# Kernel optimization log

Measured on AMD Instinct MI355X. Metric: run time of the kernel, lower is better.

The kernel has to match this reference:

```python
import jax, jax.numpy as jnp
import numpy as np

N = 8192
D_IN = 512
D_OUT = 64
ALPHA = 0.2  # LeakyReLU negative slope
MASK_VAL = -9e15


def setup_inputs() -> dict:
    key = jax.random.key(0)
    k1, k2, k3, k4 = jax.random.split(key, 4)
    inp = jax.random.normal(k1, (N, D_IN), dtype=jnp.float32)
    adj = (jax.random.uniform(k2, (N, N)) < 0.05).astype(jnp.float32)
    adj = adj.at[jnp.arange(N), jnp.arange(N)].set(1.0)
    W = jax.random.normal(k3, (D_IN, D_OUT), dtype=jnp.float32) * 0.05
    a = jax.random.normal(k4, (2 * D_OUT, 1), dtype=jnp.float32) * 0.05
    return {"input": inp, "adj": adj, "W": W, "a": a}


def reference(input, adj, W, a):
    # h = input @ W : [n, out]
    h = input @ W
    # Algebraic equivalent of the dense pairwise concat:
    # e_ij = leakyrelu([h_i || h_j] . a) = leakyrelu(h_i.a1 + h_j.a2)
    a1, a2 = a[:D_OUT, 0], a[D_OUT:, 0]          # [out], [out]
    e = jax.nn.leaky_relu(
        (h @ a1)[:, None] + (h @ a2)[None, :],    # [n, n]
        negative_slope=ALPHA,
    )
    attention = jnp.where(adj > 0, e, MASK_VAL)
    attention = jax.nn.softmax(attention, axis=1)
    out = attention @ h                            # [n, out]
    return jax.nn.elu(out)                         # end=False branch
```

## Files before the change

kernel.cpp:

```cpp
#include <hip/hip_runtime.h>
#include <hip/hip_bf16.h>

#define N 8192
#define D_IN 512
#define D_OUT 64
#define ALPHA 0.2f
#define BM 64
#define NSPLIT 4
#define KSEG (N / NSPLIT)
#define NSH (KSEG / 128)
#define NSLICE (NSPLIT * 4)

typedef __attribute__((ext_vector_type(4))) float f32x4;
typedef __attribute__((ext_vector_type(8))) short bf16x8;

static __device__ __forceinline__ unsigned pk_bf16(float lo, float hi) {
    unsigned ulo = __bfloat16_as_ushort(__float2bfloat16(lo));
    unsigned uhi = __bfloat16_as_ushort(__float2bfloat16(hi));
    return (uhi << 16) | ulo;
}

__global__ __launch_bounds__(256) void gat_mask_kernel(
    const float* __restrict__ adj, unsigned char* __restrict__ msk)
{
    size_t wave = ((size_t)blockIdx.x * 256 + threadIdx.x) >> 6;
    int lane = threadIdx.x & 63;
#pragma unroll
    for (int it = 0; it < 8; ++it) {
        size_t fo = (wave * 8 + it) * 512 + (size_t)lane * 8;
        float4 v0 = *(const float4*)(adj + fo);
        float4 v1 = *(const float4*)(adj + fo + 4);
        unsigned b =  (unsigned)(v0.x > 0.f)
                   | ((unsigned)(v0.y > 0.f) << 1)
                   | ((unsigned)(v0.z > 0.f) << 2)
                   | ((unsigned)(v0.w > 0.f) << 3)
                   | ((unsigned)(v1.x > 0.f) << 4)
                   | ((unsigned)(v1.y > 0.f) << 5)
                   | ((unsigned)(v1.z > 0.f) << 6)
                   | ((unsigned)(v1.w > 0.f) << 7);
        msk[fo >> 3] = (unsigned char)b;
    }
}

__global__ __launch_bounds__(256) void gat_h_kernel(
    const float* __restrict__ input, const float* __restrict__ W,
    const float* __restrict__ a, unsigned short* __restrict__ hpk,
    float* __restrict__ s1, float* __restrict__ s2)
{
    __shared__ float hp[4][4][64];
    int ws   = threadIdx.x >> 6;
    int lane = threadIdx.x & 63;
    int row0 = blockIdx.x * 4;
    const float* in0 = input + (size_t)row0 * D_IN + ws * 128;
    const float* Wp  = W + ws * 128 * D_OUT;
    float acc[4] = {0.f, 0.f, 0.f, 0.f};
#pragma unroll 4
    for (int k = 0; k < 128; ++k) {
        float wk = Wp[k * D_OUT + lane];
#pragma unroll
        for (int r = 0; r < 4; ++r)
            acc[r] = fmaf(in0[r * D_IN + k], wk, acc[r]);
    }
#pragma unroll
    for (int r = 0; r < 4; ++r) hp[ws][r][lane] = acc[r];
    __syncthreads();
    if (ws == 0) {
        float h[4];
#pragma unroll
        for (int r = 0; r < 4; ++r)
            h[r] = (hp[0][r][lane] + hp[1][r][lane]) + (hp[2][r][lane] + hp[3][r][lane]);
        int kw = row0 >> 5, kb = (row0 >> 3) & 3, e0 = row0 & 7;
        int dw = lane >> 4, dd = lane & 15;
        size_t off = ((size_t)((kw * 4 + dw) * 64) + kb * 16 + dd) * 8 + e0;
        uint2 hv;
        hv.x = pk_bf16(h[0], h[1]);
        hv.y = pk_bf16(h[2], h[3]);
        *(uint2*)(hpk + off) = hv;
        float a1 = a[lane], a2 = a[D_OUT + lane];
#pragma unroll
        for (int r = 0; r < 4; ++r) {
            float p1 = h[r] * a1;
            float p2 = h[r] * a2;
#pragma unroll
            for (int off2 = 32; off2; off2 >>= 1) {
                p1 += __shfl_xor(p1, off2, 64);
                p2 += __shfl_xor(p2, off2, 64);
            }
            if (lane == 0) { s1[row0 + r] = p1; s2[row0 + r] = p2; }
        }
    }
}

struct MSP { unsigned m[4]; float4 sA, sB; };
struct UBP { uint4 b0, b1, b2, b3; };

static __device__ __forceinline__ void issue_ms(MSP& p,
    const unsigned char* m0, const unsigned char* m1,
    const unsigned char* m2, const unsigned char* m3,
    const float* sb, int ps) {
    p.m[0] = m0[ps * 16];
    p.m[1] = m1[ps * 16];
    p.m[2] = m2[ps * 16];
    p.m[3] = m3[ps * 16];
    p.sA = *(const float4*)(sb + ps * 128);
    p.sB = *(const float4*)(sb + ps * 128 + 4);
}
static __device__ __forceinline__ void issue_ub(UBP& p, const unsigned short* hb,
                                                int ps) {
    const unsigned short* f = hb + ((size_t)ps << 13);
    p.b0 = *(const uint4*)(f);
    p.b1 = *(const uint4*)(f + 512);
    p.b2 = *(const uint4*)(f + 1024);
    p.b3 = *(const uint4*)(f + 1536);
}

__global__ __launch_bounds__(256, 2) void gat_flash_kernel(
    const unsigned char* __restrict__ msk, const unsigned short* __restrict__ hpk,
    const float* __restrict__ s1, const float* __restrict__ s2,
    float* __restrict__ pacc, float* __restrict__ plsum)
{
    const int tid  = threadIdx.x;
    const int lane = tid & 63;
    const int ws   = tid >> 6;
    const int i    = lane & 15;
    const int kb   = lane >> 4;
    const int hf   = blockIdx.x >> 7;
    const int rb   = blockIdx.x & 127;
    const int r0   = rb * BM;

    const unsigned char* mb0 = msk + ((size_t)(r0 +  0 + i) << 10) + hf * 256 + ws * 4 + kb;
    const unsigned char* mb1 = msk + ((size_t)(r0 + 16 + i) << 10) + hf * 256 + ws * 4 + kb;
    const unsigned char* mb2 = msk + ((size_t)(r0 + 32 + i) << 10) + hf * 256 + ws * 4 + kb;
    const unsigned char* mb3 = msk + ((size_t)(r0 + 48 + i) << 10) + hf * 256 + ws * 4 + kb;
    const float* s2b = s2 + hf * KSEG + ws * 32 + kb * 8;
    const unsigned short* hb = hpk + (((size_t)(hf * 64 + ws)) << 11) + (lane << 3);

    float eref[4];
#pragma unroll
    for (int ag = 0; ag < 4; ++ag) {
        int rg = r0 + ag * 16 + i;
        float e = s1[rg] + s2[rg];
        eref[ag] = e > 0.f ? e : ALPHA * e;
    }
    float s1r[4];
#pragma unroll
    for (int ag = 0; ag < 4; ++ag) s1r[ag] = s1[r0 + ag * 16 + i];

    float lsum[4] = {0.f, 0.f, 0.f, 0.f};
    f32x4 acc[4][4];
#pragma unroll
    for (int ag = 0; ag < 4; ++ag)
#pragma unroll
        for (int dw = 0; dw < 4; ++dw) acc[ag][dw] = f32x4{0.f, 0.f, 0.f, 0.f};

    auto step = [&](const MSP& p, const UBP& u) {
        const float* sv0 = (const float*)&p.sA;
        const float* sv1 = (const float*)&p.sB;
        const uint4 ub[4] = {u.b0, u.b1, u.b2, u.b3};
#pragma unroll
        for (int ag = 0; ag < 4; ++ag) {
            float w[8];
#pragma unroll
            for (int z = 0; z < 4; ++z) {
                float e0 = s1r[ag] + sv0[z]; e0 = e0 > 0.f ? e0 : ALPHA * e0;
                float e1 = s1r[ag] + sv1[z]; e1 = e1 > 0.f ? e1 : ALPHA * e1;
                float w0 = __expf(e0 - eref[ag]);
                float w1 = __expf(e1 - eref[ag]);
                w[z]     = ((p.m[ag] >> z) & 1u)       ? w0 : 0.f;
                w[z + 4] = ((p.m[ag] >> (z + 4)) & 1u) ? w1 : 0.f;
            }
#pragma unroll
            for (int z = 0; z < 8; ++z) lsum[ag] += w[z];
            uint4 pk;
            pk.x = pk_bf16(w[0], w[1]); pk.y = pk_bf16(w[2], w[3]);
            pk.z = pk_bf16(w[4], w[5]); pk.w = pk_bf16(w[6], w[7]);
            bf16x8 A = __builtin_bit_cast(bf16x8, pk);
            acc[ag][0] = __builtin_amdgcn_mfma_f32_16x16x32_bf16(A, __builtin_bit_cast(bf16x8, ub[0]), acc[ag][0], 0, 0, 0);
            acc[ag][1] = __builtin_amdgcn_mfma_f32_16x16x32_bf16(A, __builtin_bit_cast(bf16x8, ub[1]), acc[ag][1], 0, 0, 0);
            acc[ag][2] = __builtin_amdgcn_mfma_f32_16x16x32_bf16(A, __builtin_bit_cast(bf16x8, ub[2]), acc[ag][2], 0, 0, 0);
            acc[ag][3] = __builtin_amdgcn_mfma_f32_16x16x32_bf16(A, __builtin_bit_cast(bf16x8, ub[3]), acc[ag][3], 0, 0, 0);
        }
    };

    MSP M0, M1; UBP U0, U1;
    issue_ms(M0, mb0, mb1, mb2, mb3, s2b, 0); issue_ub(U0, hb, 0);
    issue_ms(M1, mb0, mb1, mb2, mb3, s2b, 1); issue_ub(U1, hb, 1);
    for (int p = 0; p < NSH; p += 2) {
        step(M0, U0);
        if (p + 2 < NSH) { issue_ms(M0, mb0, mb1, mb2, mb3, s2b, p + 2); issue_ub(U0, hb, p + 2); }
        step(M1, U1);
        if (p + 3 < NSH) { issue_ms(M1, mb0, mb1, mb2, mb3, s2b, p + 3); issue_ub(U1, hb, p + 3); }
    }

#pragma unroll
    for (int ag = 0; ag < 4; ++ag) {
        lsum[ag] += __shfl_xor(lsum[ag], 16, 64);
        lsum[ag] += __shfl_xor(lsum[ag], 32, 64);
    }
    const int sp = hf * 4 + ws;
    if (lane < 16) {
#pragma unroll
        for (int ag = 0; ag < 4; ++ag)
            plsum[(size_t)sp * N + r0 + ag * 16 + lane] = lsum[ag];
    }
#pragma unroll
    for (int ag = 0; ag < 4; ++ag)
#pragma unroll
        for (int dw = 0; dw < 4; ++dw)
#pragma unroll
            for (int reg = 0; reg < 4; ++reg)
                pacc[((size_t)sp * N + r0 + ag * 16 + kb * 4 + reg) * 64 + dw * 16 + i]
                    = acc[ag][dw][reg];
}

__global__ __launch_bounds__(256) void gat_reduce_kernel(
    const float* __restrict__ pacc, const float* __restrict__ plsum,
    float* __restrict__ out)
{
    int idx = blockIdx.x * 256 + threadIdx.x;
    int row = idx >> 6;
    float aa = 0.f, l = 0.f;
#pragma unroll
    for (int sp = 0; sp < NSLICE; ++sp) {
        aa += pacc[(size_t)sp * N * 64 + idx];
        l  += plsum[(size_t)sp * N + row];
    }
    float o = aa / l;
    out[idx] = o > 0.f ? o : expm1f(o);
}

extern "C" void kernel_launch(void* const* d_in, const int* in_sizes, int n_in,
                              void* d_out, int out_size, void* d_ws, size_t ws_size,
                              hipStream_t stream) {
    const float* input = (const float*)d_in[0];
    const float* adj   = (const float*)d_in[1];
    const float* W     = (const float*)d_in[2];
    const float* a     = (const float*)d_in[3];
    float* out = (float*)d_out;

    unsigned short* hpk = (unsigned short*)d_ws;
    float* s1    = (float*)(hpk + (size_t)N * D_OUT);
    float* s2    = s1 + N;
    float* pacc  = s2 + N;
    float* plsum = pacc + (size_t)NSLICE * N * 64;
    unsigned char* msk = (unsigned char*)(plsum + (size_t)NSLICE * N);

    gat_mask_kernel<<<4096, 256, 0, stream>>>(adj, msk);
    gat_h_kernel<<<2048, 256, 0, stream>>>(input, W, a, hpk, s1, s2);
    gat_flash_kernel<<<128 * NSPLIT, 256, 0, stream>>>(msk, hpk, s1, s2, pacc, plsum);
    gat_reduce_kernel<<<N * 64 / 256, 256, 0, stream>>>(pacc, plsum, out);
}
```

Before: 139.9 us.

## Halve flash row tile, reduce wave partials in LDS, batch mask loads

Shrinks the attention row tile from 64 to 32 rows, doubling the flash grid and raising launch-bound occupancy to 4 blocks per CU. The four per-wave partial accumulators are now summed in shared memory before writing, which cuts partial-sum traffic and the reduce kernel's work from 16 slices to 4. The mask kernel issues all its adjacency loads before computing and writes the mask bytes coalesced. The trade-off is that every block reloads the same h and s2 data for half as many rows, so h traffic through cache doubles, and the block gains an LDS barrier.

Result: slower. 188.7 us (+34.9%).

```diff
diff --git a/kernel.cpp b/kernel.cpp
--- a/kernel.cpp
+++ b/kernel.cpp
@@ -5,11 +5,11 @@
 #define D_IN 512
 #define D_OUT 64
 #define ALPHA 0.2f
-#define BM 64
+#define BM 32
+#define NRB (N / BM)
 #define NSPLIT 4
 #define KSEG (N / NSPLIT)
 #define NSH (KSEG / 128)
-#define NSLICE (NSPLIT * 4)
 
 typedef __attribute__((ext_vector_type(4))) float f32x4;
 typedef __attribute__((ext_vector_type(8))) short bf16x8;
@@ -25,11 +25,17 @@
 {
     size_t wave = ((size_t)blockIdx.x * 256 + threadIdx.x) >> 6;
     int lane = threadIdx.x & 63;
+    const float* base = adj + wave * 4096 + (size_t)lane * 8;
+    float4 v[16];
 #pragma unroll
     for (int it = 0; it < 8; ++it) {
-        size_t fo = (wave * 8 + it) * 512 + (size_t)lane * 8;
-        float4 v0 = *(const float4*)(adj + fo);
-        float4 v1 = *(const float4*)(adj + fo + 4);
+        v[2 * it]     = *(const float4*)(base + it * 512);
+        v[2 * it + 1] = *(const float4*)(base + it * 512 + 4);
+    }
+    size_t bo = wave * 512 + lane;
+#pragma unroll
+    for (int it = 0; it < 8; ++it) {
+        float4 v0 = v[2 * it], v1 = v[2 * it + 1];
         unsigned b =  (unsigned)(v0.x > 0.f)
                    | ((unsigned)(v0.y > 0.f) << 1)
                    | ((unsigned)(v0.z > 0.f) << 2)
@@ -38,7 +44,7 @@
                    | ((unsigned)(v1.y > 0.f) << 5)
                    | ((unsigned)(v1.z > 0.f) << 6)
                    | ((unsigned)(v1.w > 0.f) << 7);
-        msk[fo >> 3] = (unsigned char)b;
+        msk[bo + it * 64] = (unsigned char)b;
     }
 }
 
@@ -91,74 +97,67 @@
     }
 }
 
-struct MSP { unsigned m[4]; float4 sA, sB; };
+struct SSP { float4 sA, sB; };
 struct UBP { uint4 b0, b1, b2, b3; };
 
-static __device__ __forceinline__ void issue_ms(MSP& p,
-    const unsigned char* m0, const unsigned char* m1,
-    const unsigned char* m2, const unsigned char* m3,
-    const float* sb, int ps) {
-    p.m[0] = m0[ps * 16];
-    p.m[1] = m1[ps * 16];
-    p.m[2] = m2[ps * 16];
-    p.m[3] = m3[ps * 16];
-    p.sA = *(const float4*)(sb + ps * 128);
-    p.sB = *(const float4*)(sb + ps * 128 + 4);
-}
-static __device__ __forceinline__ void issue_ub(UBP& p, const unsigned short* hb,
-                                                int ps) {
-    const unsigned short* f = hb + ((size_t)ps << 13);
-    p.b0 = *(const uint4*)(f);
-    p.b1 = *(const uint4*)(f + 512);
-    p.b2 = *(const uint4*)(f + 1024);
-    p.b3 = *(const uint4*)(f + 1536);
-}
-
-__global__ __launch_bounds__(256, 2) void gat_flash_kernel(
+__global__ __launch_bounds__(256, 4) void gat_flash_kernel(
     const unsigned char* __restrict__ msk, const unsigned short* __restrict__ hpk,
     const float* __restrict__ s1, const float* __restrict__ s2,
     float* __restrict__ pacc, float* __restrict__ plsum)
 {
+    __shared__ float Cl[4][BM][D_OUT];
+    __shared__ float lsl[4][BM];
+
     const int tid  = threadIdx.x;
     const int lane = tid & 63;
     const int ws   = tid >> 6;
     const int i    = lane & 15;
     const int kb   = lane >> 4;
-    const int hf   = blockIdx.x >> 7;
-    const int rb   = blockIdx.x & 127;
+    const int hf   = blockIdx.x >> 8;
+    const int rb   = blockIdx.x & 255;
     const int r0   = rb * BM;
 
-    const unsigned char* mb0 = msk + ((size_t)(r0 +  0 + i) << 10) + hf * 256 + ws * 4 + kb;
-    const unsigned char* mb1 = msk + ((size_t)(r0 + 16 + i) << 10) + hf * 256 + ws * 4 + kb;
-    const unsigned char* mb2 = msk + ((size_t)(r0 + 32 + i) << 10) + hf * 256 + ws * 4 + kb;
-    const unsigned char* mb3 = msk + ((size_t)(r0 + 48 + i) << 10) + hf * 256 + ws * 4 + kb;
+    const unsigned char* mb = msk + ((size_t)(r0 + i) << 10) + hf * 256 + ws * 4 + kb;
     const float* s2b = s2 + hf * KSEG + ws * 32 + kb * 8;
     const unsigned short* hb = hpk + (((size_t)(hf * 64 + ws)) << 11) + (lane << 3);
 
-    float eref[4];
-#pragma unroll
-    for (int ag = 0; ag < 4; ++ag) {
+    float s1r[2], eref[2];
+#pragma unroll
+    for (int ag = 0; ag < 2; ++ag) {
         int rg = r0 + ag * 16 + i;
-        float e = s1[rg] + s2[rg];
+        s1r[ag] = s1[rg];
+        float e = s1r[ag] + s2[rg];
         eref[ag] = e > 0.f ? e : ALPHA * e;
     }
-    float s1r[4];
-#pragma unroll
-    for (int ag = 0; ag < 4; ++ag) s1r[ag] = s1[r0 + ag * 16 + i];
-
-    float lsum[4] = {0.f, 0.f, 0.f, 0.f};
-    f32x4 acc[4][4];
-#pragma unroll
-    for (int ag = 0; ag < 4; ++ag)
+    float lsum[2] = {0.f, 0.f};
+    f32x4 acc[2][4];
+#pragma unroll
+    for (int ag = 0; ag < 2; ++ag)
 #pragma unroll
         for (int dw = 0; dw < 4; ++dw) acc[ag][dw] = f32x4{0.f, 0.f, 0.f, 0.f};
 
-    auto step = [&](const MSP& p, const UBP& u) {
+    auto issue_s = [&](SSP& p, int ps) {
+        p.sA = *(const float4*)(s2b + ps * 128);
+        p.sB = *(const float4*)(s2b + ps * 128 + 4);
+    };
+    auto issue_u = [&](UBP& p, int ps) {
+        const unsigned short* f = hb + ((size_t)ps << 13);
+        p.b0 = *(const uint4*)(f);
+        p.b1 = *(const uint4*)(f + 512);
+        p.b2 = *(const uint4*)(f + 1024);
+        p.b3 = *(const uint4*)(f + 1536);
+    };
+    auto issue_m = [&](unsigned& m0, unsigned& m1, int ps) {
+        m0 = mb[ps * 16];
+        m1 = mb[ps * 16 + 16384];
+    };
+    auto step = [&](const SSP& p, const UBP& u, unsigned m0, unsigned m1) {
         const float* sv0 = (const float*)&p.sA;
         const float* sv1 = (const float*)&p.sB;
         const uint4 ub[4] = {u.b0, u.b1, u.b2, u.b3};
-#pragma unroll
-        for (int ag = 0; ag < 4; ++ag) {
+        const unsigned mm[2] = {m0, m1};
+#pragma unroll
+        for (int ag = 0; ag < 2; ++ag) {
             float w[8];
 #pragma unroll
             for (int z = 0; z < 4; ++z) {
@@ -166,8 +165,8 @@
                 float e1 = s1r[ag] + sv1[z]; e1 = e1 > 0.f ? e1 : ALPHA * e1;
                 float w0 = __expf(e0 - eref[ag]);
                 float w1 = __expf(e1 - eref[ag]);
-                w[z]     = ((p.m[ag] >> z) & 1u)       ? w0 : 0.f;
-                w[z + 4] = ((p.m[ag] >> (z + 4)) & 1u) ? w1 : 0.f;
+                w[z]     = ((mm[ag] >> z) & 1u)       ? w0 : 0.f;
+                w[z + 4] = ((mm[ag] >> (z + 4)) & 1u) ? w1 : 0.f;
             }
 #pragma unroll
             for (int z = 0; z < 8; ++z) lsum[ag] += w[z];
@@ -182,35 +181,44 @@
         }
     };
 
-    MSP M0, M1; UBP U0, U1;
-    issue_ms(M0, mb0, mb1, mb2, mb3, s2b, 0); issue_ub(U0, hb, 0);
-    issue_ms(M1, mb0, mb1, mb2, mb3, s2b, 1); issue_ub(U1, hb, 1);
+    SSP S0, S1; UBP U0, U1;
+    unsigned m0a, m0b, m1a, m1b;
+    issue_s(S0, 0); issue_u(U0, 0); issue_m(m0a, m0b, 0);
+    issue_s(S1, 1); issue_u(U1, 1); issue_m(m1a, m1b, 1);
     for (int p = 0; p < NSH; p += 2) {
-        step(M0, U0);
-        if (p + 2 < NSH) { issue_ms(M0, mb0, mb1, mb2, mb3, s2b, p + 2); issue_ub(U0, hb, p + 2); }
-        step(M1, U1);
-        if (p + 3 < NSH) { issue_ms(M1, mb0, mb1, mb2, mb3, s2b, p + 3); issue_ub(U1, hb, p + 3); }
-    }
-
-#pragma unroll
-    for (int ag = 0; ag < 4; ++ag) {
+        step(S0, U0, m0a, m0b);
+        if (p + 2 < NSH) { issue_s(S0, p + 2); issue_u(U0, p + 2); issue_m(m0a, m0b, p + 2); }
+        step(S1, U1, m1a, m1b);
+        if (p + 3 < NSH) { issue_s(S1, p + 3); issue_u(U1, p + 3); issue_m(m1a, m1b, p + 3); }
+    }
+
+#pragma unroll
+    for (int ag = 0; ag < 2; ++ag) {
         lsum[ag] += __shfl_xor(lsum[ag], 16, 64);
         lsum[ag] += __shfl_xor(lsum[ag], 32, 64);
     }
-    const int sp = hf * 4 + ws;
     if (lane < 16) {
-#pragma unroll
-        for (int ag = 0; ag < 4; ++ag)
-            plsum[(size_t)sp * N + r0 + ag * 16 + lane] = lsum[ag];
-    }
-#pragma unroll
-    for (int ag = 0; ag < 4; ++ag)
+        lsl[ws][lane]      = lsum[0];
+        lsl[ws][16 + lane] = lsum[1];
+    }
+#pragma unroll
+    for (int ag = 0; ag < 2; ++ag)
 #pragma unroll
         for (int dw = 0; dw < 4; ++dw)
 #pragma unroll
             for (int reg = 0; reg < 4; ++reg)
-                pacc[((size_t)sp * N + r0 + ag * 16 + kb * 4 + reg) * 64 + dw * 16 + i]
-                    = acc[ag][dw][reg];
+                Cl[ws][ag * 16 + kb * 4 + reg][dw * 16 + i] = acc[ag][dw][reg];
+    __syncthreads();
+
+#pragma unroll
+    for (int o = tid; o < BM * D_OUT; o += 256) {
+        int row = o >> 6, d = o & 63;
+        float v = (Cl[0][row][d] + Cl[1][row][d]) + (Cl[2][row][d] + Cl[3][row][d]);
+        pacc[((size_t)hf * N + r0 + row) * 64 + d] = v;
+    }
+    if (tid < BM)
+        plsum[hf * N + r0 + tid] =
+            (lsl[0][tid] + lsl[1][tid]) + (lsl[2][tid] + lsl[3][tid]);
 }
 
 __global__ __launch_bounds__(256) void gat_reduce_kernel(
@@ -221,9 +229,9 @@
     int row = idx >> 6;
     float aa = 0.f, l = 0.f;
 #pragma unroll
-    for (int sp = 0; sp < NSLICE; ++sp) {
-        aa += pacc[(size_t)sp * N * 64 + idx];
-        l  += plsum[(size_t)sp * N + row];
+    for (int hf = 0; hf < NSPLIT; ++hf) {
+        aa += pacc[(size_t)hf * N * 64 + idx];
+        l  += plsum[hf * N + row];
     }
     float o = aa / l;
     out[idx] = o > 0.f ? o : expm1f(o);
@@ -242,11 +250,11 @@
     float* s1    = (float*)(hpk + (size_t)N * D_OUT);
     float* s2    = s1 + N;
     float* pacc  = s2 + N;
-    float* plsum = pacc + (size_t)NSLICE * N * 64;
-    unsigned char* msk = (unsigned char*)(plsum + (size_t)NSLICE * N);
+    float* plsum = pacc + (size_t)NSPLIT * N * 64;
+    unsigned char* msk = (unsigned char*)(plsum + (size_t)NSPLIT * N);
 
     gat_mask_kernel<<<4096, 256, 0, stream>>>(adj, msk);
     gat_h_kernel<<<2048, 256, 0, stream>>>(input, W, a, hpk, s1, s2);
-    gat_flash_kernel<<<128 * NSPLIT, 256, 0, stream>>>(msk, hpk, s1, s2, pacc, plsum);
+    gat_flash_kernel<<<NRB * NSPLIT, 256, 0, stream>>>(msk, hpk, s1, s2, pacc, plsum);
     gat_reduce_kernel<<<N * 64 / 256, 256, 0, stream>>>(pacc, plsum, out);
 }
```
